# Optimization experiments

Measured on AMD Instinct MI355X. Metric: run time of the kernel, lower is better.

The kernel has to match this reference:

```python
import jax, jax.numpy as jnp
import numpy as np

N = 400000
C_IN = 64
C_OUT = 64
K = 27  # 3x3x3 kernel offsets
EPS = 1e-4


def _subm_conv(feat, nbr_t, W):
    # feat: [N, Cin], nbr_t: [K, N] int32, W: [K, Cin, Cout]
    # rulebook-style gather-GEMM-scatter: accumulate over kernel offsets
    def body(acc, kw):
        Wk, idxk = kw
        return acc + feat[idxk] @ Wk, None
    init = jnp.zeros((feat.shape[0], W.shape[-1]), feat.dtype)
    out, _ = jax.lax.scan(body, init, (W, nbr_t))
    return out


def _bn(x, g, b):
    # BatchNorm1d with track_running_stats=False: always uses batch stats
    m = x.mean(axis=0)
    v = x.var(axis=0)
    return (x - m) * jax.lax.rsqrt(v + EPS) * g + b


def _lrelu(x, slope):
    return jnp.where(x >= 0, x, slope * x)


def setup_inputs() -> dict:
    key = jax.random.key(0)
    ks = jax.random.split(key, 11)
    features = jax.random.normal(ks[0], (N, C_IN), dtype=jnp.float32)
    neighbor_idx = jax.random.randint(ks[1], (N, K), 0, N, dtype=jnp.int32)
    s = 0.05
    W1 = jax.random.normal(ks[2], (K, C_IN, C_OUT), dtype=jnp.float32) * s
    W2 = jax.random.normal(ks[3], (K, C_OUT, C_OUT), dtype=jnp.float32) * s
    W3 = jax.random.normal(ks[4], (K, C_OUT, C_OUT), dtype=jnp.float32) * s
    g1 = jax.random.normal(ks[5], (C_OUT,), dtype=jnp.float32) * 0.1 + 1.0
    b1 = jax.random.normal(ks[6], (C_OUT,), dtype=jnp.float32) * 0.1
    g2 = jax.random.normal(ks[7], (C_OUT,), dtype=jnp.float32) * 0.1 + 1.0
    b2 = jax.random.normal(ks[8], (C_OUT,), dtype=jnp.float32) * 0.1
    g3 = jax.random.normal(ks[9], (C_OUT,), dtype=jnp.float32) * 0.1 + 1.0
    b3 = jax.random.normal(ks[10], (C_OUT,), dtype=jnp.float32) * 0.1
    return {"features": features, "neighbor_idx": neighbor_idx,
            "W1": W1, "g1": g1, "b1": b1,
            "W2": W2, "g2": g2, "b2": b2,
            "W3": W3, "g3": g3, "b3": b3}


def reference(features, neighbor_idx, W1, g1, b1, W2, g2, b2, W3, g3, b3):
    nbr_t = neighbor_idx.T  # [K, N]
    # conv_block1: subm conv -> BN -> LeakyReLU(0.05)
    x = _lrelu(_bn(_subm_conv(features, nbr_t, W1), g1, b1), 0.05)
    res = x
    # conv_block2
    x = _lrelu(_bn(_subm_conv(x, nbr_t, W2), g2, b2), 0.05)
    # conv_block3 (no activation) + norm
    x = _bn(_subm_conv(x, nbr_t, W3), g3, b3)
    # residual add + scn.LeakyReLU (default leakiness = 1/3)
    return _lrelu(x + res, 0.333)
```

## Files before the change

### kernel.cpp

```cpp
#include <hip/hip_runtime.h>
#include <hip/hip_bf16.h>

#define N_PTS 400000
#define KOFF 27

typedef __attribute__((ext_vector_type(8))) short short8;
typedef __attribute__((ext_vector_type(4))) float float4v;

__device__ __forceinline__ unsigned short f2bf(float f) {
    union { float f; unsigned int u; } a; a.f = f;
    unsigned int u = a.u;
    unsigned int r = (u + 0x7FFFu + ((u >> 16) & 1u)) >> 16;
    return (unsigned short)r;
}

__device__ __forceinline__ float bf2f(unsigned short u) {
    union { unsigned int u; float f; } a; a.u = ((unsigned int)u) << 16;
    return a.f;
}

__global__ void cast_feat_kernel(const float* __restrict__ src,
                                 unsigned short* __restrict__ dst, int n4) {
    int i = blockIdx.x * blockDim.x + threadIdx.x;
    if (i >= n4) return;
    const float4* s4 = (const float4*)src;
    float4 v = s4[i];
    ushort4 o;
    o.x = f2bf(v.x); o.y = f2bf(v.y); o.z = f2bf(v.z); o.w = f2bf(v.w);
    ((ushort4*)dst)[i] = o;
}

__global__ void prep_w_kernel(const float* __restrict__ W,
                              unsigned short* __restrict__ Wt) {
    int i = blockIdx.x * blockDim.x + threadIdx.x;
    if (i >= KOFF * 64 * 64) return;
    int k = i >> 12;
    int co = (i >> 6) & 63;
    int ci = i & 63;
    Wt[i] = f2bf(W[(k << 12) + (ci << 6) + co]);
}

#define LDS_PITCH 72
__global__ __launch_bounds__(256)
void conv_kernel(const unsigned short* __restrict__ X,
                 const int* __restrict__ nbr,
                 const unsigned short* __restrict__ Wt,
                 float* __restrict__ Y,
                 float* __restrict__ stats) {
    __shared__ unsigned short lds_a[64 * LDS_PITCH];
    __shared__ unsigned short lds_w[64 * LDS_PITCH];
    const int tid = threadIdx.x;
    const int wave = tid >> 6;
    const int lane = tid & 63;
    const int quad = lane >> 4;
    const int l16 = lane & 15;
    const int p0 = blockIdx.x * 64;

    if (blockIdx.x == 0 && tid < 128) stats[tid] = 0.0f;

    const int sr = tid >> 2;
    const int sq = tid & 3;

    float4v acc[4];
    #pragma unroll
    for (int t = 0; t < 4; ++t) acc[t] = (float4v){0.f, 0.f, 0.f, 0.f};

    const int a_base = (wave * 16 + l16) * LDS_PITCH + quad * 8;

    for (int k = 0; k < KOFF; ++k) {
        __syncthreads();
        int gi = nbr[(p0 + sr) * KOFF + k];
        const uint4* srcA = (const uint4*)(X + ((size_t)gi << 6));
        uint4 a0 = srcA[sq * 2];
        uint4 a1 = srcA[sq * 2 + 1];
        uint4* dstA = (uint4*)(lds_a + sr * LDS_PITCH + sq * 16);
        dstA[0] = a0;
        dstA[1] = a1;
        const uint4* srcW = (const uint4*)(Wt + ((size_t)k << 12));
        uint4 w0 = srcW[tid];
        uint4 w1 = srcW[tid + 256];
        {
            int r0 = tid >> 3, c0 = (tid & 7) << 3;
            int r1 = (tid + 256) >> 3;
            *(uint4*)(lds_w + r0 * LDS_PITCH + c0) = w0;
            *(uint4*)(lds_w + r1 * LDS_PITCH + c0) = w1;
        }
        __syncthreads();
        #pragma unroll
        for (int ks = 0; ks < 2; ++ks) {
            short8 afrag = *(const short8*)(lds_a + a_base + ks * 32);
            #pragma unroll
            for (int t = 0; t < 4; ++t) {
                short8 bfrag = *(const short8*)(lds_w + (t * 16 + l16) * LDS_PITCH + ks * 32 + quad * 8);
                acc[t] = __builtin_amdgcn_mfma_f32_16x16x32_bf16(afrag, bfrag, acc[t], 0, 0, 0);
            }
        }
    }
    const int row_base = p0 + wave * 16 + quad * 4;
    #pragma unroll
    for (int t = 0; t < 4; ++t) {
        #pragma unroll
        for (int r = 0; r < 4; ++r) {
            Y[(size_t)(row_base + r) * 64 + t * 16 + l16] = acc[t][r];
        }
    }
}

__global__ void reduce_kernel(const float* __restrict__ Y, float* __restrict__ stats) {
    __shared__ float lsum[256], lsq[256];
    int tid = threadIdx.x;
    int c = tid & 63;
    int g = tid >> 6;
    float s = 0.f, ss = 0.f;
    for (int r = blockIdx.x * 4 + g; r < N_PTS; r += gridDim.x * 4) {
        float v = Y[(size_t)r * 64 + c];
        s += v;
        ss += v * v;
    }
    lsum[tid] = s;
    lsq[tid] = ss;
    __syncthreads();
    if (tid < 64) {
        s = lsum[tid] + lsum[tid + 64] + lsum[tid + 128] + lsum[tid + 192];
        ss = lsq[tid] + lsq[tid + 64] + lsq[tid + 128] + lsq[tid + 192];
        atomicAdd(&stats[c], s);
        atomicAdd(&stats[64 + c], ss);
    }
}

__global__ void bnact_kernel(const float* __restrict__ Y, const float* __restrict__ stats,
                             const float* __restrict__ g, const float* __restrict__ b,
                             unsigned short* __restrict__ Xb, float slope) {
    __shared__ float scale[64], shift[64];
    int tid = threadIdx.x;
    if (tid < 64) {
        float m = stats[tid] * (1.0f / N_PTS);
        float v = stats[64 + tid] * (1.0f / N_PTS) - m * m;
        float rs = rsqrtf(v + 1e-4f);
        float sc = rs * g[tid];
        scale[tid] = sc;
        shift[tid] = b[tid] - m * sc;
    }
    __syncthreads();
    int i = blockIdx.x * blockDim.x + tid;
    const int total = N_PTS * 16;
    if (i >= total) return;
    int cb = (i & 15) << 2;
    float4 y = ((const float4*)Y)[i];
    float o0 = y.x * scale[cb] + shift[cb];
    float o1 = y.y * scale[cb + 1] + shift[cb + 1];
    float o2 = y.z * scale[cb + 2] + shift[cb + 2];
    float o3 = y.w * scale[cb + 3] + shift[cb + 3];
    o0 = o0 >= 0.f ? o0 : slope * o0;
    o1 = o1 >= 0.f ? o1 : slope * o1;
    o2 = o2 >= 0.f ? o2 : slope * o2;
    o3 = o3 >= 0.f ? o3 : slope * o3;
    ushort4 o;
    o.x = f2bf(o0); o.y = f2bf(o1); o.z = f2bf(o2); o.w = f2bf(o3);
    ((ushort4*)Xb)[i] = o;
}

__global__ void bnact_final_kernel(float* __restrict__ Y, const float* __restrict__ stats,
                                   const float* __restrict__ g, const float* __restrict__ b,
                                   const unsigned short* __restrict__ res) {
    __shared__ float scale[64], shift[64];
    int tid = threadIdx.x;
    if (tid < 64) {
        float m = stats[tid] * (1.0f / N_PTS);
        float v = stats[64 + tid] * (1.0f / N_PTS) - m * m;
        float rs = rsqrtf(v + 1e-4f);
        float sc = rs * g[tid];
        scale[tid] = sc;
        shift[tid] = b[tid] - m * sc;
    }
    __syncthreads();
    int i = blockIdx.x * blockDim.x + tid;
    const int total = N_PTS * 16;
    if (i >= total) return;
    int cb = (i & 15) << 2;
    float4 y = ((const float4*)Y)[i];
    ushort4 r4 = ((const ushort4*)res)[i];
    float o0 = y.x * scale[cb] + shift[cb] + bf2f(r4.x);
    float o1 = y.y * scale[cb + 1] + shift[cb + 1] + bf2f(r4.y);
    float o2 = y.z * scale[cb + 2] + shift[cb + 2] + bf2f(r4.z);
    float o3 = y.w * scale[cb + 3] + shift[cb + 3] + bf2f(r4.w);
    o0 = o0 >= 0.f ? o0 : 0.333f * o0;
    o1 = o1 >= 0.f ? o1 : 0.333f * o1;
    o2 = o2 >= 0.f ? o2 : 0.333f * o2;
    o3 = o3 >= 0.f ? o3 : 0.333f * o3;
    float4 o; o.x = o0; o.y = o1; o.z = o2; o.w = o3;
    ((float4*)Y)[i] = o;
}

extern "C" void kernel_launch(void* const* d_in, const int* in_sizes, int n_in,
                              void* d_out, int out_size, void* d_ws, size_t ws_size,
                              hipStream_t stream) {
    const float* feat = (const float*)d_in[0];
    const int* nbr = (const int*)d_in[1];
    const float* W1 = (const float*)d_in[2];
    const float* g1 = (const float*)d_in[3];
    const float* b1 = (const float*)d_in[4];
    const float* W2 = (const float*)d_in[5];
    const float* g2 = (const float*)d_in[6];
    const float* b2 = (const float*)d_in[7];
    const float* W3 = (const float*)d_in[8];
    const float* g3 = (const float*)d_in[9];
    const float* b3 = (const float*)d_in[10];
    float* Y = (float*)d_out;

    char* ws = (char*)d_ws;
    const size_t BF_BYTES = (size_t)N_PTS * 64 * 2;
    unsigned short* B0 = (unsigned short*)ws;
    unsigned short* B1 = (unsigned short*)(ws + BF_BYTES);
    unsigned short* Wt = (unsigned short*)(ws + 2 * BF_BYTES);
    float* stats = (float*)(ws + 2 * BF_BYTES + (size_t)3 * KOFF * 4096 * 2);

    const int WSTRIDE = KOFF * 4096;

    cast_feat_kernel<<<25000, 256, 0, stream>>>(feat, B0, N_PTS * 16);
    prep_w_kernel<<<(KOFF * 4096 + 255) / 256, 256, 0, stream>>>(W1, Wt);
    prep_w_kernel<<<(KOFF * 4096 + 255) / 256, 256, 0, stream>>>(W2, Wt + WSTRIDE);
    prep_w_kernel<<<(KOFF * 4096 + 255) / 256, 256, 0, stream>>>(W3, Wt + 2 * WSTRIDE);

    conv_kernel<<<N_PTS / 64, 256, 0, stream>>>(B0, nbr, Wt, Y, stats);
    reduce_kernel<<<512, 256, 0, stream>>>(Y, stats);
    bnact_kernel<<<25000, 256, 0, stream>>>(Y, stats, g1, b1, B1, 0.05f);
    conv_kernel<<<N_PTS / 64, 256, 0, stream>>>(B1, nbr, Wt + WSTRIDE, Y, stats);
    reduce_kernel<<<512, 256, 0, stream>>>(Y, stats);
    bnact_kernel<<<25000, 256, 0, stream>>>(Y, stats, g2, b2, B0, 0.05f);
    conv_kernel<<<N_PTS / 64, 256, 0, stream>>>(B0, nbr, Wt + 2 * WSTRIDE, Y, stats);
    reduce_kernel<<<512, 256, 0, stream>>>(Y, stats);
    bnact_final_kernel<<<25000, 256, 0, stream>>>(Y, stats, g3, b3, B1);
}
```

Measured before the change: 1.201 ms.

## Fuse BN statistics into conv, prefetch gathers, enlarge conv blocks

New measurement: 1.001 ms. 1.2x faster.

```diff
diff --git a/kernel.cpp b/kernel.cpp
--- a/kernel.cpp
+++ b/kernel.cpp
@@ -3,6 +3,7 @@
 
 #define N_PTS 400000
 #define KOFF 27
+#define AP 72
 
 typedef __attribute__((ext_vector_type(8))) short short8;
 typedef __attribute__((ext_vector_type(4))) float float4v;
@@ -30,72 +31,84 @@
     ((ushort4*)dst)[i] = o;
 }
 
-__global__ void prep_w_kernel(const float* __restrict__ W,
-                              unsigned short* __restrict__ Wt) {
+__global__ void prep_w_all_kernel(const float* __restrict__ W1,
+                                  const float* __restrict__ W2,
+                                  const float* __restrict__ W3,
+                                  unsigned short* __restrict__ Wt,
+                                  float* __restrict__ stats) {
     int i = blockIdx.x * blockDim.x + threadIdx.x;
+    if (i < 384) stats[i] = 0.0f;
     if (i >= KOFF * 64 * 64) return;
     int k = i >> 12;
     int co = (i >> 6) & 63;
     int ci = i & 63;
-    Wt[i] = f2bf(W[(k << 12) + (ci << 6) + co]);
-}
-
-#define LDS_PITCH 72
-__global__ __launch_bounds__(256)
+    int src = (k << 12) + (ci << 6) + co;
+    const int WS = KOFF * 4096;
+    Wt[i] = f2bf(W1[src]);
+    Wt[i + WS] = f2bf(W2[src]);
+    Wt[i + 2 * WS] = f2bf(W3[src]);
+}
+
+__global__ __launch_bounds__(512, 6)
 void conv_kernel(const unsigned short* __restrict__ X,
                  const int* __restrict__ nbr,
                  const unsigned short* __restrict__ Wt,
                  float* __restrict__ Y,
                  float* __restrict__ stats) {
-    __shared__ unsigned short lds_a[64 * LDS_PITCH];
-    __shared__ unsigned short lds_w[64 * LDS_PITCH];
+    __shared__ unsigned short lds_a[128 * AP];
+    __shared__ unsigned short lds_w[64 * AP];
     const int tid = threadIdx.x;
     const int wave = tid >> 6;
     const int lane = tid & 63;
     const int quad = lane >> 4;
     const int l16 = lane & 15;
-    const int p0 = blockIdx.x * 64;
-
-    if (blockIdx.x == 0 && tid < 128) stats[tid] = 0.0f;
+    const int p0 = blockIdx.x * 128;
 
     const int sr = tid >> 2;
     const int sq = tid & 3;
+    const int wr = tid >> 3;
+    const int wc = (tid & 7) << 3;
 
     float4v acc[4];
     #pragma unroll
     for (int t = 0; t < 4; ++t) acc[t] = (float4v){0.f, 0.f, 0.f, 0.f};
 
-    const int a_base = (wave * 16 + l16) * LDS_PITCH + quad * 8;
+    const long nb = (long)(p0 + sr) * KOFF;
+    int gi = nbr[nb];
+    int gin = nbr[nb + 1];
+    uint4 a0, a1, w0;
+    {
+        const uint4* srcA = (const uint4*)(X + ((size_t)gi << 6)) + sq * 2;
+        a0 = srcA[0];
+        a1 = srcA[1];
+        w0 = ((const uint4*)Wt)[tid];
+    }
 
     for (int k = 0; k < KOFF; ++k) {
         __syncthreads();
-        int gi = nbr[(p0 + sr) * KOFF + k];
-        const uint4* srcA = (const uint4*)(X + ((size_t)gi << 6));
-        uint4 a0 = srcA[sq * 2];
-        uint4 a1 = srcA[sq * 2 + 1];
-        uint4* dstA = (uint4*)(lds_a + sr * LDS_PITCH + sq * 16);
-        dstA[0] = a0;
-        dstA[1] = a1;
-        const uint4* srcW = (const uint4*)(Wt + ((size_t)k << 12));
-        uint4 w0 = srcW[tid];
-        uint4 w1 = srcW[tid + 256];
-        {
-            int r0 = tid >> 3, c0 = (tid & 7) << 3;
-            int r1 = (tid + 256) >> 3;
-            *(uint4*)(lds_w + r0 * LDS_PITCH + c0) = w0;
-            *(uint4*)(lds_w + r1 * LDS_PITCH + c0) = w1;
+        *(uint4*)(lds_a + sr * AP + sq * 16) = a0;
+        *(uint4*)(lds_a + sr * AP + sq * 16 + 8) = a1;
+        *(uint4*)(lds_w + wr * AP + wc) = w0;
+        if (k < KOFF - 1) {
+            const uint4* srcA = (const uint4*)(X + ((size_t)gin << 6)) + sq * 2;
+            a0 = srcA[0];
+            a1 = srcA[1];
+            w0 = ((const uint4*)(Wt + (((size_t)(k + 1)) << 12)))[tid];
+            gin = (k < KOFF - 2) ? nbr[nb + k + 2] : 0;
         }
         __syncthreads();
+        const int abase = (wave * 16 + l16) * AP + quad * 8;
         #pragma unroll
         for (int ks = 0; ks < 2; ++ks) {
-            short8 afrag = *(const short8*)(lds_a + a_base + ks * 32);
+            short8 af = *(const short8*)(lds_a + abase + ks * 32);
             #pragma unroll
             for (int t = 0; t < 4; ++t) {
-                short8 bfrag = *(const short8*)(lds_w + (t * 16 + l16) * LDS_PITCH + ks * 32 + quad * 8);
-                acc[t] = __builtin_amdgcn_mfma_f32_16x16x32_bf16(afrag, bfrag, acc[t], 0, 0, 0);
+                short8 bf = *(const short8*)(lds_w + (t * 16 + l16) * AP + ks * 32 + quad * 8);
+                acc[t] = __builtin_amdgcn_mfma_f32_16x16x32_bf16(af, bf, acc[t], 0, 0, 0);
             }
         }
     }
+
     const int row_base = p0 + wave * 16 + quad * 4;
     #pragma unroll
     for (int t = 0; t < 4; ++t) {
@@ -104,28 +117,27 @@
             Y[(size_t)(row_base + r) * 64 + t * 16 + l16] = acc[t][r];
         }
     }
-}
-
-__global__ void reduce_kernel(const float* __restrict__ Y, float* __restrict__ stats) {
-    __shared__ float lsum[256], lsq[256];
-    int tid = threadIdx.x;
-    int c = tid & 63;
-    int g = tid >> 6;
-    float s = 0.f, ss = 0.f;
-    for (int r = blockIdx.x * 4 + g; r < N_PTS; r += gridDim.x * 4) {
-        float v = Y[(size_t)r * 64 + c];
-        s += v;
-        ss += v * v;
-    }
-    lsum[tid] = s;
-    lsq[tid] = ss;
-    __syncthreads();
-    if (tid < 64) {
-        s = lsum[tid] + lsum[tid + 64] + lsum[tid + 128] + lsum[tid + 192];
-        ss = lsq[tid] + lsq[tid + 64] + lsq[tid + 128] + lsq[tid + 192];
-        atomicAdd(&stats[c], s);
-        atomicAdd(&stats[64 + c], ss);
-    }
+
+    __syncthreads();
+    float* red = (float*)lds_w;
+    if (tid < 128) red[tid] = 0.0f;
+    __syncthreads();
+    #pragma unroll
+    for (int t = 0; t < 4; ++t) {
+        float s = acc[t][0] + acc[t][1] + acc[t][2] + acc[t][3];
+        float ss = acc[t][0] * acc[t][0] + acc[t][1] * acc[t][1] +
+                   acc[t][2] * acc[t][2] + acc[t][3] * acc[t][3];
+        s += __shfl_down(s, 32);
+        s += __shfl_down(s, 16);
+        ss += __shfl_down(ss, 32);
+        ss += __shfl_down(ss, 16);
+        if (lane < 16) {
+            atomicAdd(&red[t * 16 + l16], s);
+            atomicAdd(&red[64 + t * 16 + l16], ss);
+        }
+    }
+    __syncthreads();
+    if (tid < 128) atomicAdd(&stats[tid], red[tid]);
 }
 
 __global__ void bnact_kernel(const float* __restrict__ Y, const float* __restrict__ stats,
@@ -218,17 +230,12 @@
     const int WSTRIDE = KOFF * 4096;
 
     cast_feat_kernel<<<25000, 256, 0, stream>>>(feat, B0, N_PTS * 16);
-    prep_w_kernel<<<(KOFF * 4096 + 255) / 256, 256, 0, stream>>>(W1, Wt);
-    prep_w_kernel<<<(KOFF * 4096 + 255) / 256, 256, 0, stream>>>(W2, Wt + WSTRIDE);
-    prep_w_kernel<<<(KOFF * 4096 + 255) / 256, 256, 0, stream>>>(W3, Wt + 2 * WSTRIDE);
-
-    conv_kernel<<<N_PTS / 64, 256, 0, stream>>>(B0, nbr, Wt, Y, stats);
-    reduce_kernel<<<512, 256, 0, stream>>>(Y, stats);
+    prep_w_all_kernel<<<(KOFF * 4096 + 255) / 256, 256, 0, stream>>>(W1, W2, W3, Wt, stats);
+
+    conv_kernel<<<N_PTS / 128, 512, 0, stream>>>(B0, nbr, Wt, Y, stats);
     bnact_kernel<<<25000, 256, 0, stream>>>(Y, stats, g1, b1, B1, 0.05f);
-    conv_kernel<<<N_PTS / 64, 256, 0, stream>>>(B1, nbr, Wt + WSTRIDE, Y, stats);
-    reduce_kernel<<<512, 256, 0, stream>>>(Y, stats);
-    bnact_kernel<<<25000, 256, 0, stream>>>(Y, stats, g2, b2, B0, 0.05f);
-    conv_kernel<<<N_PTS / 64, 256, 0, stream>>>(B0, nbr, Wt + 2 * WSTRIDE, Y, stats);
-    reduce_kernel<<<512, 256, 0, stream>>>(Y, stats);
-    bnact_final_kernel<<<25000, 256, 0, stream>>>(Y, stats, g3, b3, B1);
-}
+    conv_kernel<<<N_PTS / 128, 512, 0, stream>>>(B1, nbr, Wt + WSTRIDE, Y, stats + 128);
+    bnact_kernel<<<25000, 256, 0, stream>>>(Y, stats + 128, g2, b2, B0, 0.05f);
+    conv_kernel<<<N_PTS / 128, 512, 0, stream>>>(B0, nbr, Wt + 2 * WSTRIDE, Y, stats + 256);
+    bnact_final_kernel<<<25000, 256, 0, stream>>>(Y, stats + 256, g3, b3, B1);
+}
```
